# Optimization experiments

Hardware: AMD Instinct MI355X
Metric: run time of the kernel (lower is better)

## Reference

```python
import jax, jax.numpy as jnp
import numpy as np

N, E, IN, ED, HID, HEADS, OUT, G = 50000, 800000, 128, 16, 32, 4, 64, 64
NEG_SLOPE = 0.2


def gat_conv(x, src, dst, edge_attr, W, att_src, att_dst, We, att_edge, bias,
             heads, out_ch, concat):
    """PyG-style GATConv with edge attributes and mean-filled self loops.
    src/dst already include self loops; edge_attr already includes fill rows."""
    n = x.shape[0]
    h = (x @ W).reshape(n, heads, out_ch)                      # [N,H,C]
    a_src = jnp.einsum('nhc,hc->nh', h, att_src)               # [N,H]
    a_dst = jnp.einsum('nhc,hc->nh', h, att_dst)
    eh = (edge_attr @ We).reshape(-1, heads, out_ch)           # [E',H,C]
    a_edge = jnp.einsum('ehc,hc->eh', eh, att_edge)            # [E',H]
    alpha = jax.nn.leaky_relu(a_src[src] + a_dst[dst] + a_edge, NEG_SLOPE)
    # segment softmax over incoming edges of each target node
    amax = jax.ops.segment_max(alpha, dst, num_segments=n)
    ex = jnp.exp(alpha - amax[dst])
    denom = jax.ops.segment_sum(ex, dst, num_segments=n)
    coef = ex / (denom[dst] + 1e-16)                           # [E',H]
    msg = h[src] * coef[:, :, None]                            # [E',H,C]
    out = jax.ops.segment_sum(msg, dst, num_segments=n)        # [N,H,C]
    out = out.reshape(n, heads * out_ch) if concat else out.mean(axis=1)
    return out + bias


def add_self_loops(edge_index, edge_attr, n):
    loop = jnp.arange(n, dtype=edge_index.dtype)
    src = jnp.concatenate([edge_index[0], loop])
    dst = jnp.concatenate([edge_index[1], loop])
    fill = jnp.broadcast_to(edge_attr.mean(axis=0), (n, edge_attr.shape[1]))
    ea = jnp.concatenate([edge_attr, fill], axis=0)
    return src, dst, ea


def setup_inputs() -> dict:
    key = jax.random.key(0)
    ks = jax.random.split(key, 16)
    s1 = 1.0 / np.sqrt(IN)
    s2 = 1.0 / np.sqrt(HID * HEADS)
    se = 1.0 / np.sqrt(ED)
    return {
        'x': jax.random.normal(ks[0], (N, IN), jnp.float32),
        'edge_index': jax.random.randint(ks[1], (2, E), 0, N, jnp.int64),
        'edge_attr': jax.random.normal(ks[2], (E, ED), jnp.float32),
        'batch': jnp.sort(jax.random.randint(ks[3], (N,), 0, G, jnp.int64)),
        # layer 1 params (heads=4, concat=True)
        'W1': jax.random.normal(ks[4], (IN, HEADS * HID), jnp.float32) * s1,
        'att_src1': jax.random.normal(ks[5], (HEADS, HID), jnp.float32) * s1,
        'att_dst1': jax.random.normal(ks[6], (HEADS, HID), jnp.float32) * s1,
        'We1': jax.random.normal(ks[7], (ED, HEADS * HID), jnp.float32) * se,
        'att_edge1': jax.random.normal(ks[8], (HEADS, HID), jnp.float32) * se,
        'b1': jnp.zeros((HEADS * HID,), jnp.float32),
        # layer 2 params (heads=1, concat=False)
        'W2': jax.random.normal(ks[9], (HEADS * HID, OUT), jnp.float32) * s2,
        'att_src2': jax.random.normal(ks[10], (1, OUT), jnp.float32) * s2,
        'att_dst2': jax.random.normal(ks[11], (1, OUT), jnp.float32) * s2,
        'We2': jax.random.normal(ks[12], (ED, OUT), jnp.float32) * se,
        'att_edge2': jax.random.normal(ks[13], (1, OUT), jnp.float32) * se,
        'b2': jnp.zeros((OUT,), jnp.float32),
    }


def reference(x, edge_index, edge_attr, batch,
              W1, att_src1, att_dst1, We1, att_edge1, b1,
              W2, att_src2, att_dst2, We2, att_edge2, b2):
    src, dst, ea = add_self_loops(edge_index, edge_attr, x.shape[0])
    h = gat_conv(x, src, dst, ea, W1, att_src1, att_dst1, We1, att_edge1, b1,
                 HEADS, HID, concat=True)
    h = jax.nn.elu(h)
    h = gat_conv(h, src, dst, ea, W2, att_src2, att_dst2, We2, att_edge2, b2,
                 1, OUT, concat=False)
    # global mean pool over graphs
    sums = jax.ops.segment_sum(h, batch, num_segments=G)
    cnts = jax.ops.segment_sum(jnp.ones((h.shape[0],), h.dtype), batch, num_segments=G)
    return sums / jnp.maximum(cnts, 1.0)[:, None]
```

## Files before the change

kernel.cpp:

```cpp
#include <hip/hip_runtime.h>
#include <hip/hip_fp16.h>
#include <math.h>

#define NN 50000
#define NE 800000
#define EDF 16
#define C1 128
#define HID 32
#define OUTF 64
#define NG 64
#define SLOPE 0.2f
#define NB 196
#define MAXE 256
#define PB 256
#define PCH 196
#define SEB 512
#define HB 3125
#define GB1 1564

static inline int cdiv(long a, long b){ return (int)((a + b - 1) / b); }

__device__ __forceinline__ float lrelu(float x){ return x >= 0.f ? x : SLOPE * x; }

__global__ __launch_bounds__(256) void k_pre(const float* __restrict__ ea,
                                             float* __restrict__ part,
                                             const int* __restrict__ dst,
                                             int* __restrict__ deg,
                                             int* __restrict__ rank){
  int b = blockIdx.x;
  int t = threadIdx.x;
  if (b < SEB){
    const float4* ea4 = (const float4*)ea;
    const long total = (long)NE * 4;
    const long stride = (long)SEB * 256;
    float4 acc = make_float4(0.f, 0.f, 0.f, 0.f);
    for (long i = (long)b * 256 + t; i < total; i += stride * 4){
      float4 a0 = make_float4(0,0,0,0), a1 = a0, a2 = a0, a3 = a0;
      long i1 = i + stride, i2 = i + 2*stride, i3 = i + 3*stride;
      a0 = ea4[i];
      if (i1 < total) a1 = ea4[i1];
      if (i2 < total) a2 = ea4[i2];
      if (i3 < total) a3 = ea4[i3];
      acc.x += a0.x + a1.x + a2.x + a3.x;
      acc.y += a0.y + a1.y + a2.y + a3.y;
      acc.z += a0.z + a1.z + a2.z + a3.z;
      acc.w += a0.w + a1.w + a2.w + a3.w;
    }
    __shared__ float4 sp[256];
    sp[t] = acc;
    __syncthreads();
    for (int st = 128; st >= 4; st >>= 1){
      if (t < st){
        sp[t].x += sp[t+st].x; sp[t].y += sp[t+st].y;
        sp[t].z += sp[t+st].z; sp[t].w += sp[t+st].w;
      }
      __syncthreads();
    }
    if (t < 4) *(float4*)&part[b * 16 + t * 4] = sp[t];
  } else {
    long e = (long)(b - SEB) * 256 + t;
    if (e < NE) rank[e] = atomicAdd(&deg[dst[e]], 1);
  }
}

__global__ void k_scan1(const int* __restrict__ deg, int* __restrict__ rowStart,
                        int* __restrict__ blockSums,
                        const float* __restrict__ We1, const float* __restrict__ att_e1,
                        const float* __restrict__ We2, const float* __restrict__ att_e2,
                        const float* __restrict__ part,
                        float* __restrict__ M1, float* __restrict__ M2,
                        float* __restrict__ aeSL1, float* __restrict__ aeSL2){
  int t = threadIdx.x;
  if (blockIdx.x == NB){
    __shared__ float sMean[16];
    __shared__ float sM1p[64];
    if (t < 64){
      int h = t >> 4, d = t & 15;
      float s = 0.f;
      for (int c = 0; c < HID; c++) s += We1[d * C1 + h * HID + c] * att_e1[h * HID + c];
      M1[h * 16 + d] = s; sM1p[t] = s;
    }
    __shared__ float sM2p[16];
    if (t >= 64 && t < 80){
      int d = t - 64;
      float s = 0.f;
      for (int c = 0; c < OUTF; c++) s += We2[d * OUTF + c] * att_e2[c];
      M2[d] = s; sM2p[d] = s;
    }
    if (t >= 80 && t < 96){
      int c = t - 80;
      float s = 0.f;
      for (int b = 0; b < SEB; b++) s += part[b * 16 + c];
      sMean[c] = s * (1.0f / NE);
    }
    __syncthreads();
    if (t < 4){
      float s = 0.f;
      for (int d = 0; d < 16; d++) s += sMean[d] * sM1p[t * 16 + d];
      aeSL1[t] = s;
    }
    if (t == 4){
      float s = 0.f;
      for (int d = 0; d < 16; d++) s += sMean[d] * sM2p[d];
      *aeSL2 = s;
    }
    return;
  }
  __shared__ int sd[256];
  int i = blockIdx.x * 256 + t;
  int v = (i < NN) ? deg[i] : 0;
  sd[t] = v;
  __syncthreads();
  for (int off = 1; off < 256; off <<= 1){
    int add = (t >= off) ? sd[t - off] : 0;
    __syncthreads();
    sd[t] += add;
    __syncthreads();
  }
  int incl = sd[t];
  if (i < NN) rowStart[i] = incl - v;
  if (t == 255) blockSums[blockIdx.x] = incl;
}

__global__ void k_scan3(int* __restrict__ rowStart, const int* __restrict__ blockSums){
  __shared__ int sp[256];
  int t = threadIdx.x;
  int bid = blockIdx.x;
  sp[t] = (t < bid) ? blockSums[t] : 0;
  __syncthreads();
  for (int st = 128; st >= 1; st >>= 1){
    if (t < st) sp[t] += sp[t + st];
    __syncthreads();
  }
  int prefix = sp[0];
  int i = bid * 256 + t;
  if (i < NN) rowStart[i] += prefix;
  if (i == 0) rowStart[NN] = NE;
}

__global__ __launch_bounds__(256) void k_sg(
    const int* __restrict__ src, const int* __restrict__ dst,
    const float* __restrict__ ea, const int* __restrict__ rowStart,
    const int* __restrict__ rank,
    const float* __restrict__ M1, const float* __restrict__ M2,
    unsigned int* __restrict__ recC,
    const float* __restrict__ A, const float* __restrict__ B,
    __half* __restrict__ Ch, const float* __restrict__ attS,
    const float* __restrict__ attD,
    float* __restrict__ aS, float* __restrict__ aD){
  __shared__ float As[16][64];
  __shared__ float Bs[16][64];
  __shared__ float sM[80];
  int t = threadIdx.x;
  if (blockIdx.x >= GB1){
    if (t < 64) sM[t] = M1[t];
    if (t >= 64 && t < 80) sM[t] = M2[t - 64];
    __syncthreads();
    long e = (long)(blockIdx.x - GB1) * 256 + t;
    if (e >= NE) return;
    int d = dst[e];
    int s = src[e];
    int rk = rank[e];
    float eav[16];
    const float4* p = (const float4*)(ea + e * EDF);
    *(float4*)&eav[0]  = p[0]; *(float4*)&eav[4]  = p[1];
    *(float4*)&eav[8]  = p[2]; *(float4*)&eav[12] = p[3];
    int pos = rowStart[d] + rk;
    float ae[4];
#pragma unroll
    for (int h = 0; h < 4; h++){
      float sdot = 0.f;
#pragma unroll
      for (int dd = 0; dd < 16; dd++) sdot += eav[dd] * sM[h * 16 + dd];
      ae[h] = sdot;
    }
    float a2 = 0.f;
#pragma unroll
    for (int dd = 0; dd < 16; dd++) a2 += eav[dd] * sM[64 + dd];
    __half2 ae01 = __floats2half2_rn(ae[0], ae[1]);
    __half2 ae23 = __floats2half2_rn(ae[2], ae[3]);
    __half  a2h  = __float2half_rn(a2);
    uint4 rec;
    rec.x = (unsigned)s | ((unsigned)*(unsigned short*)&a2h << 16);
    rec.y = *(unsigned*)&ae01;
    rec.z = *(unsigned*)&ae23;
    rec.w = 0u;
    *(uint4*)&recC[(long)pos * 4] = rec;
    return;
  }
  const int M = NN, Ncols = C1, K = 128;
  int bg = blockIdx.x;
  int row0 = (bg >> 1) * 64, col0 = (bg & 1) * 64;
  int tx = t & 15, ty = t >> 4;
  int lrow = t >> 2, lkq = t & 3;
  int bk = t >> 4, bc = t & 15;
  float acc[4][4] = {};
  for (int k0 = 0; k0 < K; k0 += 16){
    float4 a4 = make_float4(0.f, 0.f, 0.f, 0.f);
    int gr = row0 + lrow;
    if (gr < M) a4 = *(const float4*)&A[(long)gr * K + k0 + lkq * 4];
    As[lkq * 4 + 0][lrow] = a4.x; As[lkq * 4 + 1][lrow] = a4.y;
    As[lkq * 4 + 2][lrow] = a4.z; As[lkq * 4 + 3][lrow] = a4.w;
    *(float4*)&Bs[bk][bc * 4] = *(const float4*)&B[(long)(k0 + bk) * Ncols + col0 + bc * 4];
    __syncthreads();
#pragma unroll
    for (int k = 0; k < 16; k++){
      float4 a = *(float4*)&As[k][ty * 4];
      float4 b = *(float4*)&Bs[k][tx * 4];
      acc[0][0] += a.x*b.x; acc[0][1] += a.x*b.y; acc[0][2] += a.x*b.z; acc[0][3] += a.x*b.w;
      acc[1][0] += a.y*b.x; acc[1][1] += a.y*b.y; acc[1][2] += a.y*b.z; acc[1][3] += a.y*b.w;
      acc[2][0] += a.z*b.x; acc[2][1] += a.z*b.y; acc[2][2] += a.z*b.z; acc[2][3] += a.z*b.w;
      acc[3][0] += a.w*b.x; acc[3][1] += a.w*b.y; acc[3][2] += a.w*b.z; acc[3][3] += a.w*b.w;
    }
    __syncthreads();
  }
#pragma unroll
  for (int i = 0; i < 4; i++){
    int r = row0 + ty * 4 + i;
    if (r < M){
      __half2 p0 = __floats2half2_rn(acc[i][0], acc[i][1]);
      __half2 p1 = __floats2half2_rn(acc[i][2], acc[i][3]);
      uint2 pk; pk.x = *(unsigned*)&p0; pk.y = *(unsigned*)&p1;
      *(uint2*)&Ch[(long)r * Ncols + col0 + tx * 4] = pk;
    }
  }
  float4 avS = *(const float4*)&attS[col0 + tx * 4];
  float4 avD = *(const float4*)&attD[col0 + tx * 4];
  float ss[4], sd[4];
#pragma unroll
  for (int i = 0; i < 4; i++){
    ss[i] = acc[i][0]*avS.x + acc[i][1]*avS.y + acc[i][2]*avS.z + acc[i][3]*avS.w;
    sd[i] = acc[i][0]*avD.x + acc[i][1]*avD.y + acc[i][2]*avD.z + acc[i][3]*avD.w;
  }
#pragma unroll
  for (int off = 1; off <= 4; off <<= 1){
#pragma unroll
    for (int i = 0; i < 4; i++){
      ss[i] += __shfl_xor(ss[i], off);
      sd[i] += __shfl_xor(sd[i], off);
    }
  }
  if ((tx & 7) == 0){
    int head = (bg & 1) * 2 + (tx >> 3);
#pragma unroll
    for (int i = 0; i < 4; i++){
      int r = row0 + ty * 4 + i;
      if (r < M){ aS[(long)r * 4 + head] = ss[i]; aD[(long)r * 4 + head] = sd[i]; }
    }
  }
}

__global__ __launch_bounds__(256) void k_gemm2(const __half* __restrict__ Ah,
                                               const float* __restrict__ B,
                                               __half* __restrict__ Ch,
                                               const float* __restrict__ attS,
                                               const float* __restrict__ attD,
                                               float* __restrict__ aS, float* __restrict__ aD){
  __shared__ float As[16][64];
  __shared__ float Bs[16][64];
  const int M = NN, Ncols = OUTF, K = 128;
  int tid = threadIdx.x;
  int row0 = blockIdx.x * 64, col0 = 0;
  int tx = tid & 15, ty = tid >> 4;
  int lrow = tid >> 2, lkq = tid & 3;
  int bk = tid >> 4, bc = tid & 15;
  float acc[4][4] = {};
  for (int k0 = 0; k0 < K; k0 += 16){
    float4 a4 = make_float4(0.f, 0.f, 0.f, 0.f);
    int gr = row0 + lrow;
    if (gr < M){
      uint2 u = *(const uint2*)&Ah[(long)gr * K + k0 + lkq * 4];
      float2 f0 = __half22float2(*(__half2*)&u.x);
      float2 f1 = __half22float2(*(__half2*)&u.y);
      a4 = make_float4(f0.x, f0.y, f1.x, f1.y);
    }
    As[lkq * 4 + 0][lrow] = a4.x; As[lkq * 4 + 1][lrow] = a4.y;
    As[lkq * 4 + 2][lrow] = a4.z; As[lkq * 4 + 3][lrow] = a4.w;
    *(float4*)&Bs[bk][bc * 4] = *(const float4*)&B[(long)(k0 + bk) * Ncols + col0 + bc * 4];
    __syncthreads();
#pragma unroll
    for (int k = 0; k < 16; k++){
      float4 a = *(float4*)&As[k][ty * 4];
      float4 b = *(float4*)&Bs[k][tx * 4];
      acc[0][0] += a.x*b.x; acc[0][1] += a.x*b.y; acc[0][2] += a.x*b.z; acc[0][3] += a.x*b.w;
      acc[1][0] += a.y*b.x; acc[1][1] += a.y*b.y; acc[1][2] += a.y*b.z; acc[1][3] += a.y*b.w;
      acc[2][0] += a.z*b.x; acc[2][1] += a.z*b.y; acc[2][2] += a.z*b.z; acc[2][3] += a.z*b.w;
      acc[3][0] += a.w*b.x; acc[3][1] += a.w*b.y; acc[3][2] += a.w*b.z; acc[3][3] += a.w*b.w;
    }
    __syncthreads();
  }
#pragma unroll
  for (int i = 0; i < 4; i++){
    int r = row0 + ty * 4 + i;
    if (r < M){
      __half2 p0 = __floats2half2_rn(acc[i][0], acc[i][1]);
      __half2 p1 = __floats2half2_rn(acc[i][2], acc[i][3]);
      uint2 pk; pk.x = *(unsigned*)&p0; pk.y = *(unsigned*)&p1;
      *(uint2*)&Ch[(long)r * Ncols + tx * 4] = pk;
    }
  }
  float4 avS = *(const float4*)&attS[tx * 4];
  float4 avD = *(const float4*)&attD[tx * 4];
  float ss[4], sd[4];
#pragma unroll
  for (int i = 0; i < 4; i++){
    ss[i] = acc[i][0]*avS.x + acc[i][1]*avS.y + acc[i][2]*avS.z + acc[i][3]*avS.w;
    sd[i] = acc[i][0]*avD.x + acc[i][1]*avD.y + acc[i][2]*avD.z + acc[i][3]*avD.w;
  }
#pragma unroll
  for (int off = 1; off <= 8; off <<= 1){
#pragma unroll
    for (int i = 0; i < 4; i++){
      ss[i] += __shfl_xor(ss[i], off);
      sd[i] += __shfl_xor(sd[i], off);
    }
  }
  if (tx == 0){
#pragma unroll
    for (int i = 0; i < 4; i++){
      int r = row0 + ty * 4 + i;
      if (r < M){ aS[r] = ss[i]; aD[r] = sd[i]; }
    }
  }
}

__global__ __launch_bounds__(256) void k_agg1(
    const int* __restrict__ rowStart, const unsigned int* __restrict__ recC,
    const float* __restrict__ a_src, const float* __restrict__ a_dst,
    const float* __restrict__ aeSL1,
    const __half* __restrict__ h1h, const float* __restrict__ b1,
    __half* __restrict__ out1h){
  __shared__ int   sS[4][MAXE];
  __shared__ float sC[4][MAXE * 4];
  int wid = threadIdx.x >> 6;
  int lane = threadIdx.x & 63;
  int n = blockIdx.x * 4 + wid;
  int start = rowStart[n];
  int dg = rowStart[n + 1] - start;
  float4 sl4 = *(const float4*)aeSL1;
  float4 ad4 = *(const float4*)(a_dst + (long)n * 4);
  float4 as4 = *(const float4*)(a_src + (long)n * 4);
  float4 cSelf;
  cSelf.x = __expf(lrelu(as4.x + ad4.x + sl4.x));
  cSelf.y = __expf(lrelu(as4.y + ad4.y + sl4.y));
  cSelf.z = __expf(lrelu(as4.z + ad4.z + sl4.z));
  cSelf.w = __expf(lrelu(as4.w + ad4.w + sl4.w));
  float4 dsum = make_float4(0.f, 0.f, 0.f, 0.f);
  for (int j0 = 0; j0 < dg; j0 += 64){
    int j = j0 + lane;
    if (j < dg){
      uint4 rec = *(const uint4*)&recC[(long)(start + j) * 4];
      int s = rec.x & 0xffff;
      float2 ae01 = __half22float2(*(__half2*)&rec.y);
      float2 ae23 = __half22float2(*(__half2*)&rec.z);
      float4 asv = *(const float4*)(a_src + (long)s * 4);
      float4 c;
      c.x = __expf(lrelu(asv.x + ad4.x + ae01.x));
      c.y = __expf(lrelu(asv.y + ad4.y + ae01.y));
      c.z = __expf(lrelu(asv.z + ad4.z + ae23.x));
      c.w = __expf(lrelu(asv.w + ad4.w + ae23.y));
      dsum.x += c.x; dsum.y += c.y; dsum.z += c.z; dsum.w += c.w;
      if (j < MAXE){
        sS[wid][j] = s << 6;
        *(float4*)&sC[wid][j * 4] = c;
      }
    }
  }
#pragma unroll
  for (int off = 32; off > 0; off >>= 1){
    dsum.x += __shfl_xor(dsum.x, off);
    dsum.y += __shfl_xor(dsum.y, off);
    dsum.z += __shfl_xor(dsum.z, off);
    dsum.w += __shfl_xor(dsum.w, off);
  }
  float adA[4] = {ad4.x, ad4.y, ad4.z, ad4.w};
  float csA[4] = {cSelf.x, cSelf.y, cSelf.z, cSelf.w};
  float invA[4];
  invA[0] = 1.f / (dsum.x + cSelf.x + 1e-16f);
  invA[1] = 1.f / (dsum.y + cSelf.y + 1e-16f);
  invA[2] = 1.f / (dsum.z + cSelf.z + 1e-16f);
  invA[3] = 1.f / (dsum.w + cSelf.w + 1e-16f);
  int ch = lane * 2;
  int h = lane >> 4;
  const unsigned int* hrow = (const unsigned int*)h1h;
  float cs   = csA[h];
  float vinv = invA[h];
  float adh  = adA[h];
  unsigned int hv = hrow[(unsigned)(n * 64 + lane)];
  float2 hf = __half22float2(*(__half2*)&hv);
  float acc0 = hf.x * cs, acc1 = hf.y * cs;
  int jmax = dg < MAXE ? dg : MAXE;
  int j = 0;
  for (; j + 4 <= jmax; j += 4){
    int o0 = sS[wid][j+0], o1 = sS[wid][j+1], o2 = sS[wid][j+2], o3 = sS[wid][j+3];
    float c0 = sC[wid][(j+0)*4+h], c1 = sC[wid][(j+1)*4+h];
    float c2 = sC[wid][(j+2)*4+h], c3 = sC[wid][(j+3)*4+h];
    unsigned int v0 = hrow[(unsigned)(o0 + lane)];
    unsigned int v1 = hrow[(unsigned)(o1 + lane)];
    unsigned int v2 = hrow[(unsigned)(o2 + lane)];
    unsigned int v3 = hrow[(unsigned)(o3 + lane)];
    float2 f0 = __half22float2(*(__half2*)&v0);
    float2 f1 = __half22float2(*(__half2*)&v1);
    float2 f2 = __half22float2(*(__half2*)&v2);
    float2 f3 = __half22float2(*(__half2*)&v3);
    acc0 += c0 * f0.x + c1 * f1.x + c2 * f2.x + c3 * f3.x;
    acc1 += c0 * f0.y + c1 * f1.y + c2 * f2.y + c3 * f3.y;
  }
  for (; j < jmax; j++){
    int o = sS[wid][j];
    float c = sC[wid][j * 4 + h];
    unsigned int v = hrow[(unsigned)(o + lane)];
    float2 f = __half22float2(*(__half2*)&v);
    acc0 += c * f.x; acc1 += c * f.y;
  }
  for (; j < dg; j++){
    uint4 rec = *(const uint4*)&recC[(long)(start + j) * 4];
    int s = rec.x & 0xffff;
    float2 ae01 = __half22float2(*(__half2*)&rec.y);
    float2 ae23 = __half22float2(*(__half2*)&rec.z);
    float aeA[4] = {ae01.x, ae01.y, ae23.x, ae23.y};
    float asv = a_src[(long)s * 4 + h];
    float c = __expf(lrelu(asv + adh + aeA[h]));
    unsigned int v = hrow[(unsigned)((s << 6) + lane)];
    float2 f = __half22float2(*(__half2*)&v);
    acc0 += c * f.x; acc1 += c * f.y;
  }
  float v0 = acc0 * vinv + b1[ch];
  float v1 = acc1 * vinv + b1[ch + 1];
  v0 = v0 > 0.f ? v0 : __expf(v0) - 1.f;
  v1 = v1 > 0.f ? v1 : __expf(v1) - 1.f;
  __half2 pk = __floats2half2_rn(v0, v1);
  ((unsigned int*)out1h)[(unsigned)(n * 64 + lane)] = *(unsigned*)&pk;
}

__global__ __launch_bounds__(256) void k_agg2(
    const int* __restrict__ rowStart, const unsigned int* __restrict__ recC,
    const float* __restrict__ a_src, const float* __restrict__ a_dst,
    const float* __restrict__ aeSL2,
    const __half* __restrict__ h2h, float* __restrict__ out2){
  __shared__ int   sS[4][MAXE];
  __shared__ float sC[4][MAXE];
  int wid = threadIdx.x >> 6;
  int lane = threadIdx.x & 63;
  int n = blockIdx.x * 4 + wid;
  int start = rowStart[n];
  int dg = rowStart[n + 1] - start;
  float adN = a_dst[n];
  float cSelf = __expf(lrelu(a_src[n] + adN + *aeSL2));
  float dsum = 0.f;
  for (int j0 = 0; j0 < dg; j0 += 64){
    int j = j0 + lane;
    if (j < dg){
      unsigned rx = recC[(long)(start + j) * 4];
      int s = rx & 0xffff;
      unsigned short ah = (unsigned short)(rx >> 16);
      float c = __expf(lrelu(a_src[s] + adN + __half2float(*(__half*)&ah)));
      dsum += c;
      if (j < MAXE){ sS[wid][j] = s << 6; sC[wid][j] = c; }
    }
  }
#pragma unroll
  for (int off = 32; off > 0; off >>= 1) dsum += __shfl_xor(dsum, off);
  float inv = 1.f / (dsum + cSelf + 1e-16f);
  float acc = __half2float(h2h[(unsigned)(n * 64 + lane)]) * cSelf;
  int jmax = dg < MAXE ? dg : MAXE;
  int j = 0;
  for (; j + 4 <= jmax; j += 4){
    int o0 = sS[wid][j+0], o1 = sS[wid][j+1], o2 = sS[wid][j+2], o3 = sS[wid][j+3];
    float c0 = sC[wid][j+0], c1 = sC[wid][j+1], c2 = sC[wid][j+2], c3 = sC[wid][j+3];
    float f0 = __half2float(h2h[(unsigned)(o0 + lane)]);
    float f1 = __half2float(h2h[(unsigned)(o1 + lane)]);
    float f2 = __half2float(h2h[(unsigned)(o2 + lane)]);
    float f3 = __half2float(h2h[(unsigned)(o3 + lane)]);
    acc += c0 * f0 + c1 * f1 + c2 * f2 + c3 * f3;
  }
  for (; j < jmax; j++)
    acc += sC[wid][j] * __half2float(h2h[(unsigned)(sS[wid][j] + lane)]);
  for (; j < dg; j++){
    unsigned rx = recC[(long)(start + j) * 4];
    int s = rx & 0xffff;
    unsigned short ah = (unsigned short)(rx >> 16);
    float c = __expf(lrelu(a_src[s] + adN + __half2float(*(__half*)&ah)));
    acc += c * __half2float(h2h[(unsigned)((s << 6) + lane)]);
  }
  out2[(long)n * OUTF + lane] = acc * inv;
}

__global__ __launch_bounds__(256) void k_pool1(const float* __restrict__ out2,
                                               const int* __restrict__ batch,
                                               float* __restrict__ gsum){
  int c = threadIdx.x & 63, r = threadIdx.x >> 6;
  int n0 = blockIdx.x * PCH + r;
  int n1 = blockIdx.x * PCH + PCH; if (n1 > NN) n1 = NN;
  float acc = 0.f; int curG = -1;
  for (int n = n0; n < n1; n += 4){
    int g = batch[n];
    if (g != curG){
      if (curG >= 0) atomicAdd(&gsum[curG * 64 + c], acc);
      curG = g; acc = 0.f;
    }
    acc += out2[(long)n * OUTF + c];
  }
  if (curG >= 0) atomicAdd(&gsum[curG * 64 + c], acc);
}

__global__ void k_pool2(const float* __restrict__ gsum, const int* __restrict__ batch,
                        const float* __restrict__ b2, float* __restrict__ out){
  int g = blockIdx.x;
  int c = threadIdx.x;
  int lo = 0, hi = NN;
  while (lo < hi){ int mid = (lo + hi) >> 1; if (batch[mid] < g) lo = mid + 1; else hi = mid; }
  int a = lo, b = NN;
  while (a < b){ int mid = (a + b) >> 1; if (batch[mid] < g + 1) a = mid + 1; else b = mid; }
  int cnt = a - lo;
  out[g * 64 + c] = (gsum[g * 64 + c] + (float)cnt * b2[c]) / fmaxf((float)cnt, 1.0f);
}

extern "C" void kernel_launch(void* const* d_in, const int* in_sizes, int n_in,
                              void* d_out, int out_size, void* d_ws, size_t ws_size,
                              hipStream_t stream) {
  const float* x         = (const float*)d_in[0];
  const int*   eidx      = (const int*)d_in[1];
  const float* edge_attr = (const float*)d_in[2];
  const int*   batch     = (const int*)d_in[3];
  const float* W1        = (const float*)d_in[4];
  const float* att_src1  = (const float*)d_in[5];
  const float* att_dst1  = (const float*)d_in[6];
  const float* We1       = (const float*)d_in[7];
  const float* att_edge1 = (const float*)d_in[8];
  const float* b1        = (const float*)d_in[9];
  const float* W2        = (const float*)d_in[10];
  const float* att_src2  = (const float*)d_in[11];
  const float* att_dst2  = (const float*)d_in[12];
  const float* We2       = (const float*)d_in[13];
  const float* att_edge2 = (const float*)d_in[14];
  const float* b2        = (const float*)d_in[15];
  const int* srcI = eidx;
  const int* dstI = eidx + NE;

  float* ws = (float*)d_ws;
  __half* h1h   = (__half*)ws;
  __half* out1h = (__half*)(ws + 3200000);
  float* out2   = ws + 6400000;
  float* a_src1 = ws + 9600000;
  float* a_dst1 = a_src1 + (long)NN * 4;
  unsigned int* recC = (unsigned int*)(a_dst1 + (long)NN * 4);
  int*   deg    = (int*)(recC + (long)NE * 4);
  float* gsum   = (float*)(deg + NN);
  int*   rowStart = (int*)(gsum + NG * 64);
  int*   blockSums = rowStart + 50004;
  float* part   = (float*)(blockSums + 260);
  float* M1     = part + SEB * 16;
  float* M2v    = M1 + 64;
  float* aeSL1  = M2v + 16;
  float* aeSL2  = aeSL1 + 4;
  int*   rank   = (int*)(aeSL2 + 4);
  __half* h2h = h1h;
  float* a_src2 = a_src1; float* a_dst2 = a_dst1;

  hipMemsetAsync(deg, 0, (NN + NG * 64) * sizeof(int), stream);
  k_pre<<<SEB + HB, 256, 0, stream>>>(edge_attr, part, dstI, deg, rank);
  k_scan1<<<NB + 1, 256, 0, stream>>>(deg, rowStart, blockSums,
                                      We1, att_edge1, We2, att_edge2, part,
                                      M1, M2v, aeSL1, aeSL2);
  k_scan3<<<NB, 256, 0, stream>>>(rowStart, blockSums);
  k_sg<<<GB1 + HB, 256, 0, stream>>>(srcI, dstI, edge_attr, rowStart, rank,
                                     M1, M2v, recC,
                                     x, W1, h1h, att_src1, att_dst1,
                                     a_src1, a_dst1);
  k_agg1<<<NN / 4, 256, 0, stream>>>(rowStart, recC, a_src1, a_dst1, aeSL1,
                                     h1h, b1, out1h);
  k_gemm2<<<dim3(cdiv(NN, 64), 1), 256, 0, stream>>>(out1h, W2, h2h, att_src2, att_dst2,
                                                     a_src2, a_dst2);
  k_agg2<<<NN / 4, 256, 0, stream>>>(rowStart, recC, a_src2, a_dst2, aeSL2,
                                     h2h, out2);
  k_pool1<<<PB, 256, 0, stream>>>(out2, batch, gsum);
  k_pool2<<<NG, 64, 0, stream>>>(gsum, batch, b2, (float*)d_out);
}
```

Baseline: 330.7 us.

## Use split-fp16 MFMA for both GAT GEMMs and separate edge-scatter kernel

Replaces the scalar fp32 SIMT GEMMs for layer 1 and layer 2 with MFMA 16x16x32 fp16 kernels. Precision is kept near fp32 by splitting operands into high and scaled low fp16 parts: three products for layer 1, two for layer 2. Weights are pre-transposed and split in extra blocks of the scan kernel, and the attention logits are fused into the GEMM epilogue. The edge record scatter previously fused with GEMM1 becomes its own kernel launch, which removes that concurrency and adds some rounding-error risk.

New measurement: 352.6 us. +6.6%, slower.

```diff
diff --git a/kernel.cpp b/kernel.cpp
--- a/kernel.cpp
+++ b/kernel.cpp
@@ -16,11 +16,16 @@
 #define PCH 196
 #define SEB 512
 #define HB 3125
-#define GB1 1564
+#define G1B 1563
+#define G2B 1563
 
 static inline int cdiv(long a, long b){ return (int)((a + b - 1) / b); }
 
 __device__ __forceinline__ float lrelu(float x){ return x >= 0.f ? x : SLOPE * x; }
+
+typedef _Float16 f16x8 __attribute__((ext_vector_type(8)));
+typedef float f32x4 __attribute__((ext_vector_type(4)));
+#define MFMA16(a, b, c) __builtin_amdgcn_mfma_f32_16x16x32_f16((a), (b), (c), 0, 0, 0)
 
 __global__ __launch_bounds__(256) void k_pre(const float* __restrict__ ea,
                                              float* __restrict__ part,
@@ -69,8 +74,31 @@
                         const float* __restrict__ We2, const float* __restrict__ att_e2,
                         const float* __restrict__ part,
                         float* __restrict__ M1, float* __restrict__ M2,
-                        float* __restrict__ aeSL1, float* __restrict__ aeSL2){
+                        float* __restrict__ aeSL1, float* __restrict__ aeSL2,
+                        const float* __restrict__ W1, const float* __restrict__ W2,
+                        __half* __restrict__ W1Th, __half* __restrict__ W1Tl,
+                        __half* __restrict__ W2Th, __half* __restrict__ W2Tl){
   int t = threadIdx.x;
+  if (blockIdx.x == NB + 1){
+    for (int i = t; i < 128 * 128; i += 256){
+      int c = i & 127, k = i >> 7;
+      float w = W1[i];
+      __half h = __float2half_rn(w);
+      W1Th[c * 128 + k] = h;
+      W1Tl[c * 128 + k] = __float2half_rn((w - __half2float(h)) * 4096.0f);
+    }
+    return;
+  }
+  if (blockIdx.x == NB + 2){
+    for (int i = t; i < 128 * 64; i += 256){
+      int c = i & 63, k = i >> 6;
+      float w = W2[i];
+      __half h = __float2half_rn(w);
+      W2Th[c * 128 + k] = h;
+      W2Tl[c * 128 + k] = __float2half_rn((w - __half2float(h)) * 4096.0f);
+    }
+    return;
+  }
   if (blockIdx.x == NB){
     __shared__ float sMean[16];
     __shared__ float sM1p[64];
@@ -138,189 +166,259 @@
   if (i == 0) rowStart[NN] = NE;
 }
 
-__global__ __launch_bounds__(256) void k_sg(
+__global__ __launch_bounds__(256) void k_gemm1(
+    const float* __restrict__ x,
+    const __half* __restrict__ W1Th, const __half* __restrict__ W1Tl,
+    __half* __restrict__ Ch,
+    const float* __restrict__ attS, const float* __restrict__ attD,
+    float* __restrict__ aS, float* __restrict__ aD){
+  __shared__ __align__(16) __half Ash[4096];
+  __shared__ __align__(16) __half Asl[4096];
+  int t = threadIdx.x;
+  int row0 = blockIdx.x * 32;
+  {
+    int srow = t >> 3, sseg = t & 7;
+    int gr = row0 + srow;
+    float xv[16];
+    if (gr < NN){
+      const float4* xp = (const float4*)(x + (long)gr * 128 + sseg * 16);
+      *(float4*)&xv[0]  = xp[0]; *(float4*)&xv[4]  = xp[1];
+      *(float4*)&xv[8]  = xp[2]; *(float4*)&xv[12] = xp[3];
+    } else {
+#pragma unroll
+      for (int i = 0; i < 16; i++) xv[i] = 0.f;
+    }
+    f16x8 vh[2], vl[2];
+#pragma unroll
+    for (int q = 0; q < 2; q++)
+#pragma unroll
+      for (int i = 0; i < 8; i++){
+        float f = xv[q * 8 + i];
+        _Float16 h = (_Float16)f;
+        vh[q][i] = h;
+        vl[q][i] = (_Float16)(f - (float)h);
+      }
+    int sb = srow * 256 + sseg * 32;
+    int sw = (srow & 7) << 4;
+    *(f16x8*)((char*)Ash + ((sb     ) ^ sw)) = vh[0];
+    *(f16x8*)((char*)Ash + ((sb + 16) ^ sw)) = vh[1];
+    *(f16x8*)((char*)Asl + ((sb     ) ^ sw)) = vl[0];
+    *(f16x8*)((char*)Asl + ((sb + 16) ^ sw)) = vl[1];
+  }
+  __syncthreads();
+  int wave = t >> 6, lane = t & 63, g = lane >> 4, li = lane & 15;
+  const f16x8* BhP = (const f16x8*)W1Th;
+  const f16x8* BlP = (const f16x8*)W1Tl;
+  int c0 = wave * 32 + li;
+  int c1 = c0 + 16;
+  f32x4 z = {0.f, 0.f, 0.f, 0.f};
+  f32x4 aM00 = z, aM01 = z, aM10 = z, aM11 = z;
+  f32x4 aL00 = z, aL01 = z, aL10 = z, aL11 = z;
+  int ro0 = li * 256, ro1 = (16 + li) * 256;
+  int sw0 = (li & 7) << 4;
+#pragma unroll
+  for (int ks = 0; ks < 4; ks++){
+    int ko = ks * 64 + g * 16;
+    f16x8 ah0 = *(const f16x8*)((char*)Ash + ((ro0 + ko) ^ sw0));
+    f16x8 ah1 = *(const f16x8*)((char*)Ash + ((ro1 + ko) ^ sw0));
+    f16x8 al0 = *(const f16x8*)((char*)Asl + ((ro0 + ko) ^ sw0));
+    f16x8 al1 = *(const f16x8*)((char*)Asl + ((ro1 + ko) ^ sw0));
+    f16x8 bh0 = BhP[c0 * 16 + ks * 4 + g];
+    f16x8 bh1 = BhP[c1 * 16 + ks * 4 + g];
+    f16x8 bl0 = BlP[c0 * 16 + ks * 4 + g];
+    f16x8 bl1 = BlP[c1 * 16 + ks * 4 + g];
+    aM00 = MFMA16(ah0, bh0, aM00); aM01 = MFMA16(ah0, bh1, aM01);
+    aM10 = MFMA16(ah1, bh0, aM10); aM11 = MFMA16(ah1, bh1, aM11);
+    aM00 = MFMA16(al0, bh0, aM00); aM01 = MFMA16(al0, bh1, aM01);
+    aM10 = MFMA16(al1, bh0, aM10); aM11 = MFMA16(al1, bh1, aM11);
+    aL00 = MFMA16(ah0, bl0, aL00); aL01 = MFMA16(ah0, bl1, aL01);
+    aL10 = MFMA16(ah1, bl0, aL10); aL11 = MFMA16(ah1, bl1, aL11);
+  }
+  const float s = 1.0f / 4096.0f;
+  f32x4 D00 = aM00 + aL00 * s, D01 = aM01 + aL01 * s;
+  f32x4 D10 = aM10 + aL10 * s, D11 = aM11 + aL11 * s;
+  float avS0 = attS[c0], avS1 = attS[c1];
+  float avD0 = attD[c0], avD1 = attD[c1];
+  float ssv[2][4], sdv[2][4];
+#pragma unroll
+  for (int r = 0; r < 4; r++){
+    ssv[0][r] = D00[r] * avS0 + D01[r] * avS1;
+    ssv[1][r] = D10[r] * avS0 + D11[r] * avS1;
+    sdv[0][r] = D00[r] * avD0 + D01[r] * avD1;
+    sdv[1][r] = D10[r] * avD0 + D11[r] * avD1;
+  }
+#pragma unroll
+  for (int off = 1; off <= 8; off <<= 1)
+#pragma unroll
+    for (int mt = 0; mt < 2; mt++)
+#pragma unroll
+      for (int r = 0; r < 4; r++){
+        ssv[mt][r] += __shfl_xor(ssv[mt][r], off);
+        sdv[mt][r] += __shfl_xor(sdv[mt][r], off);
+      }
+  __syncthreads();
+  __half* sOut = Ash;
+#pragma unroll
+  for (int mt = 0; mt < 2; mt++)
+#pragma unroll
+    for (int r = 0; r < 4; r++){
+      int rl = mt * 16 + g * 4 + r;
+      sOut[rl * 128 + c0] = __float2half_rn(mt ? D10[r] : D00[r]);
+      sOut[rl * 128 + c1] = __float2half_rn(mt ? D11[r] : D01[r]);
+    }
+  if (li == 0){
+#pragma unroll
+    for (int mt = 0; mt < 2; mt++)
+#pragma unroll
+      for (int r = 0; r < 4; r++){
+        int grow = row0 + mt * 16 + g * 4 + r;
+        if (grow < NN){
+          aS[(long)grow * 4 + wave] = ssv[mt][r];
+          aD[(long)grow * 4 + wave] = sdv[mt][r];
+        }
+      }
+  }
+  __syncthreads();
+  {
+    int row = t >> 3, seg = t & 7;
+    int grw = row0 + row;
+    if (grw < NN){
+      uint4 u0 = *(uint4*)&sOut[row * 128 + seg * 16];
+      uint4 u1 = *(uint4*)&sOut[row * 128 + seg * 16 + 8];
+      *(uint4*)&Ch[(long)grw * 128 + seg * 16] = u0;
+      *(uint4*)&Ch[(long)grw * 128 + seg * 16 + 8] = u1;
+    }
+  }
+}
+
+__global__ __launch_bounds__(256) void k_sc(
     const int* __restrict__ src, const int* __restrict__ dst,
     const float* __restrict__ ea, const int* __restrict__ rowStart,
     const int* __restrict__ rank,
     const float* __restrict__ M1, const float* __restrict__ M2,
-    unsigned int* __restrict__ recC,
-    const float* __restrict__ A, const float* __restrict__ B,
-    __half* __restrict__ Ch, const float* __restrict__ attS,
-    const float* __restrict__ attD,
-    float* __restrict__ aS, float* __restrict__ aD){
-  __shared__ float As[16][64];
-  __shared__ float Bs[16][64];
+    unsigned int* __restrict__ recC){
   __shared__ float sM[80];
   int t = threadIdx.x;
-  if (blockIdx.x >= GB1){
-    if (t < 64) sM[t] = M1[t];
-    if (t >= 64 && t < 80) sM[t] = M2[t - 64];
-    __syncthreads();
-    long e = (long)(blockIdx.x - GB1) * 256 + t;
-    if (e >= NE) return;
-    int d = dst[e];
-    int s = src[e];
-    int rk = rank[e];
-    float eav[16];
-    const float4* p = (const float4*)(ea + e * EDF);
-    *(float4*)&eav[0]  = p[0]; *(float4*)&eav[4]  = p[1];
-    *(float4*)&eav[8]  = p[2]; *(float4*)&eav[12] = p[3];
-    int pos = rowStart[d] + rk;
-    float ae[4];
-#pragma unroll
-    for (int h = 0; h < 4; h++){
-      float sdot = 0.f;
-#pragma unroll
-      for (int dd = 0; dd < 16; dd++) sdot += eav[dd] * sM[h * 16 + dd];
-      ae[h] = sdot;
-    }
-    float a2 = 0.f;
-#pragma unroll
-    for (int dd = 0; dd < 16; dd++) a2 += eav[dd] * sM[64 + dd];
-    __half2 ae01 = __floats2half2_rn(ae[0], ae[1]);
-    __half2 ae23 = __floats2half2_rn(ae[2], ae[3]);
-    __half  a2h  = __float2half_rn(a2);
-    uint4 rec;
-    rec.x = (unsigned)s | ((unsigned)*(unsigned short*)&a2h << 16);
-    rec.y = *(unsigned*)&ae01;
-    rec.z = *(unsigned*)&ae23;
-    rec.w = 0u;
-    *(uint4*)&recC[(long)pos * 4] = rec;
-    return;
-  }
-  const int M = NN, Ncols = C1, K = 128;
-  int bg = blockIdx.x;
-  int row0 = (bg >> 1) * 64, col0 = (bg & 1) * 64;
-  int tx = t & 15, ty = t >> 4;
-  int lrow = t >> 2, lkq = t & 3;
-  int bk = t >> 4, bc = t & 15;
-  float acc[4][4] = {};
-  for (int k0 = 0; k0 < K; k0 += 16){
-    float4 a4 = make_float4(0.f, 0.f, 0.f, 0.f);
-    int gr = row0 + lrow;
-    if (gr < M) a4 = *(const float4*)&A[(long)gr * K + k0 + lkq * 4];
-    As[lkq * 4 + 0][lrow] = a4.x; As[lkq * 4 + 1][lrow] = a4.y;
-    As[lkq * 4 + 2][lrow] = a4.z; As[lkq * 4 + 3][lrow] = a4.w;
-    *(float4*)&Bs[bk][bc * 4] = *(const float4*)&B[(long)(k0 + bk) * Ncols + col0 + bc * 4];
-    __syncthreads();
-#pragma unroll
-    for (int k = 0; k < 16; k++){
-      float4 a = *(float4*)&As[k][ty * 4];
-      float4 b = *(float4*)&Bs[k][tx * 4];
-      acc[0][0] += a.x*b.x; acc[0][1] += a.x*b.y; acc[0][2] += a.x*b.z; acc[0][3] += a.x*b.w;
-      acc[1][0] += a.y*b.x; acc[1][1] += a.y*b.y; acc[1][2] += a.y*b.z; acc[1][3] += a.y*b.w;
-      acc[2][0] += a.z*b.x; acc[2][1] += a.z*b.y; acc[2][2] += a.z*b.z; acc[2][3] += a.z*b.w;
-      acc[3][0] += a.w*b.x; acc[3][1] += a.w*b.y; acc[3][2] += a.w*b.z; acc[3][3] += a.w*b.w;
-    }
-    __syncthreads();
-  }
-#pragma unroll
-  for (int i = 0; i < 4; i++){
-    int r = row0 + ty * 4 + i;
-    if (r < M){
-      __half2 p0 = __floats2half2_rn(acc[i][0], acc[i][1]);
-      __half2 p1 = __floats2half2_rn(acc[i][2], acc[i][3]);
-      uint2 pk; pk.x = *(unsigned*)&p0; pk.y = *(unsigned*)&p1;
-      *(uint2*)&Ch[(long)r * Ncols + col0 + tx * 4] = pk;
-    }
-  }
-  float4 avS = *(const float4*)&attS[col0 + tx * 4];
-  float4 avD = *(const float4*)&attD[col0 + tx * 4];
-  float ss[4], sd[4];
-#pragma unroll
-  for (int i = 0; i < 4; i++){
-    ss[i] = acc[i][0]*avS.x + acc[i][1]*avS.y + acc[i][2]*avS.z + acc[i][3]*avS.w;
-    sd[i] = acc[i][0]*avD.x + acc[i][1]*avD.y + acc[i][2]*avD.z + acc[i][3]*avD.w;
-  }
-#pragma unroll
-  for (int off = 1; off <= 4; off <<= 1){
-#pragma unroll
-    for (int i = 0; i < 4; i++){
-      ss[i] += __shfl_xor(ss[i], off);
-      sd[i] += __shfl_xor(sd[i], off);
-    }
-  }
-  if ((tx & 7) == 0){
-    int head = (bg & 1) * 2 + (tx >> 3);
-#pragma unroll
-    for (int i = 0; i < 4; i++){
-      int r = row0 + ty * 4 + i;
-      if (r < M){ aS[(long)r * 4 + head] = ss[i]; aD[(long)r * 4 + head] = sd[i]; }
-    }
-  }
-}
-
-__global__ __launch_bounds__(256) void k_gemm2(const __half* __restrict__ Ah,
-                                               const float* __restrict__ B,
-                                               __half* __restrict__ Ch,
-                                               const float* __restrict__ attS,
-                                               const float* __restrict__ attD,
-                                               float* __restrict__ aS, float* __restrict__ aD){
-  __shared__ float As[16][64];
-  __shared__ float Bs[16][64];
-  const int M = NN, Ncols = OUTF, K = 128;
-  int tid = threadIdx.x;
-  int row0 = blockIdx.x * 64, col0 = 0;
-  int tx = tid & 15, ty = tid >> 4;
-  int lrow = tid >> 2, lkq = tid & 3;
-  int bk = tid >> 4, bc = tid & 15;
-  float acc[4][4] = {};
-  for (int k0 = 0; k0 < K; k0 += 16){
-    float4 a4 = make_float4(0.f, 0.f, 0.f, 0.f);
-    int gr = row0 + lrow;
-    if (gr < M){
-      uint2 u = *(const uint2*)&Ah[(long)gr * K + k0 + lkq * 4];
-      float2 f0 = __half22float2(*(__half2*)&u.x);
-      float2 f1 = __half22float2(*(__half2*)&u.y);
-      a4 = make_float4(f0.x, f0.y, f1.x, f1.y);
-    }
-    As[lkq * 4 + 0][lrow] = a4.x; As[lkq * 4 + 1][lrow] = a4.y;
-    As[lkq * 4 + 2][lrow] = a4.z; As[lkq * 4 + 3][lrow] = a4.w;
-    *(float4*)&Bs[bk][bc * 4] = *(const float4*)&B[(long)(k0 + bk) * Ncols + col0 + bc * 4];
-    __syncthreads();
-#pragma unroll
-    for (int k = 0; k < 16; k++){
-      float4 a = *(float4*)&As[k][ty * 4];
-      float4 b = *(float4*)&Bs[k][tx * 4];
-      acc[0][0] += a.x*b.x; acc[0][1] += a.x*b.y; acc[0][2] += a.x*b.z; acc[0][3] += a.x*b.w;
-      acc[1][0] += a.y*b.x; acc[1][1] += a.y*b.y; acc[1][2] += a.y*b.z; acc[1][3] += a.y*b.w;
-      acc[2][0] += a.z*b.x; acc[2][1] += a.z*b.y; acc[2][2] += a.z*b.z; acc[2][3] += a.z*b.w;
-      acc[3][0] += a.w*b.x; acc[3][1] += a.w*b.y; acc[3][2] += a.w*b.z; acc[3][3] += a.w*b.w;
-    }
-    __syncthreads();
-  }
-#pragma unroll
-  for (int i = 0; i < 4; i++){
-    int r = row0 + ty * 4 + i;
-    if (r < M){
-      __half2 p0 = __floats2half2_rn(acc[i][0], acc[i][1]);
-      __half2 p1 = __floats2half2_rn(acc[i][2], acc[i][3]);
-      uint2 pk; pk.x = *(unsigned*)&p0; pk.y = *(unsigned*)&p1;
-      *(uint2*)&Ch[(long)r * Ncols + tx * 4] = pk;
-    }
-  }
-  float4 avS = *(const float4*)&attS[tx * 4];
-  float4 avD = *(const float4*)&attD[tx * 4];
-  float ss[4], sd[4];
-#pragma unroll
-  for (int i = 0; i < 4; i++){
-    ss[i] = acc[i][0]*avS.x + acc[i][1]*avS.y + acc[i][2]*avS.z + acc[i][3]*avS.w;
-    sd[i] = acc[i][0]*avD.x + acc[i][1]*avD.y + acc[i][2]*avD.z + acc[i][3]*avD.w;
-  }
-#pragma unroll
-  for (int off = 1; off <= 8; off <<= 1){
-#pragma unroll
-    for (int i = 0; i < 4; i++){
-      ss[i] += __shfl_xor(ss[i], off);
-      sd[i] += __shfl_xor(sd[i], off);
-    }
-  }
-  if (tx == 0){
-#pragma unroll
-    for (int i = 0; i < 4; i++){
-      int r = row0 + ty * 4 + i;
-      if (r < M){ aS[r] = ss[i]; aD[r] = sd[i]; }
-    }
+  if (t < 64) sM[t] = M1[t];
+  if (t >= 64 && t < 80) sM[t] = M2[t - 64];
+  __syncthreads();
+  long e = (long)blockIdx.x * 256 + t;
+  if (e >= NE) return;
+  int d = dst[e];
+  int s = src[e];
+  int rk = rank[e];
+  float eav[16];
+  const float4* p = (const float4*)(ea + e * EDF);
+  *(float4*)&eav[0]  = p[0]; *(float4*)&eav[4]  = p[1];
+  *(float4*)&eav[8]  = p[2]; *(float4*)&eav[12] = p[3];
+  int pos = rowStart[d] + rk;
+  float ae[4];
+#pragma unroll
+  for (int h = 0; h < 4; h++){
+    float sdot = 0.f;
+#pragma unroll
+    for (int dd = 0; dd < 16; dd++) sdot += eav[dd] * sM[h * 16 + dd];
+    ae[h] = sdot;
+  }
+  float a2 = 0.f;
+#pragma unroll
+  for (int dd = 0; dd < 16; dd++) a2 += eav[dd] * sM[64 + dd];
+  __half2 ae01 = __floats2half2_rn(ae[0], ae[1]);
+  __half2 ae23 = __floats2half2_rn(ae[2], ae[3]);
+  __half  a2h  = __float2half_rn(a2);
+  uint4 rec;
+  rec.x = (unsigned)s | ((unsigned)*(unsigned short*)&a2h << 16);
+  rec.y = *(unsigned*)&ae01;
+  rec.z = *(unsigned*)&ae23;
+  rec.w = 0u;
+  *(uint4*)&recC[(long)pos * 4] = rec;
+}
+
+__global__ __launch_bounds__(256) void k_gemm2(
+    const __half* __restrict__ Ahp,
+    const __half* __restrict__ W2Th, const __half* __restrict__ W2Tl,
+    __half* __restrict__ Ch,
+    const float* __restrict__ attS, const float* __restrict__ attD,
+    float* __restrict__ aS, float* __restrict__ aD){
+  __shared__ __align__(16) __half As[4096];
+  __shared__ float sRS[128], sRD[128];
+  int t = threadIdx.x;
+  int row0 = blockIdx.x * 32;
+  {
+    int srow = t >> 3, sseg = t & 7;
+    int gr = row0 + srow;
+    uint4 u0 = {0,0,0,0}, u1 = {0,0,0,0};
+    if (gr < NN){
+      const uint4* p = (const uint4*)(Ahp + (long)gr * 128 + sseg * 16);
+      u0 = p[0]; u1 = p[1];
+    }
+    int sb = srow * 256 + sseg * 32;
+    int sw = (srow & 7) << 4;
+    *(uint4*)((char*)As + ((sb     ) ^ sw)) = u0;
+    *(uint4*)((char*)As + ((sb + 16) ^ sw)) = u1;
+  }
+  __syncthreads();
+  int wave = t >> 6, lane = t & 63, g = lane >> 4, li = lane & 15;
+  int cw = wave * 16 + li;
+  const f16x8* BhP = (const f16x8*)W2Th;
+  const f16x8* BlP = (const f16x8*)W2Tl;
+  f32x4 z = {0.f, 0.f, 0.f, 0.f};
+  f32x4 aM0 = z, aM1 = z, aL0 = z, aL1 = z;
+  int ro0 = li * 256, ro1 = (16 + li) * 256, sw0 = (li & 7) << 4;
+#pragma unroll
+  for (int ks = 0; ks < 4; ks++){
+    int ko = ks * 64 + g * 16;
+    f16x8 a0 = *(const f16x8*)((char*)As + ((ro0 + ko) ^ sw0));
+    f16x8 a1 = *(const f16x8*)((char*)As + ((ro1 + ko) ^ sw0));
+    f16x8 bh = BhP[cw * 16 + ks * 4 + g];
+    f16x8 bl = BlP[cw * 16 + ks * 4 + g];
+    aM0 = MFMA16(a0, bh, aM0); aM1 = MFMA16(a1, bh, aM1);
+    aL0 = MFMA16(a0, bl, aL0); aL1 = MFMA16(a1, bl, aL1);
+  }
+  const float s = 1.0f / 4096.0f;
+  f32x4 D0 = aM0 + aL0 * s, D1 = aM1 + aL1 * s;
+  float avS = attS[cw], avD = attD[cw];
+  float ssv[2][4], sdv[2][4];
+#pragma unroll
+  for (int r = 0; r < 4; r++){
+    ssv[0][r] = D0[r] * avS; ssv[1][r] = D1[r] * avS;
+    sdv[0][r] = D0[r] * avD; sdv[1][r] = D1[r] * avD;
+  }
+#pragma unroll
+  for (int off = 1; off <= 8; off <<= 1)
+#pragma unroll
+    for (int mt = 0; mt < 2; mt++)
+#pragma unroll
+      for (int r = 0; r < 4; r++){
+        ssv[mt][r] += __shfl_xor(ssv[mt][r], off);
+        sdv[mt][r] += __shfl_xor(sdv[mt][r], off);
+      }
+  __syncthreads();
+  __half* sOut = As;
+#pragma unroll
+  for (int mt = 0; mt < 2; mt++)
+#pragma unroll
+    for (int r = 0; r < 4; r++){
+      int rl = mt * 16 + g * 4 + r;
+      sOut[rl * 64 + cw] = __float2half_rn(mt ? D1[r] : D0[r]);
+      if (li == 0){
+        sRS[wave * 32 + rl] = ssv[mt][r];
+        sRD[wave * 32 + rl] = sdv[mt][r];
+      }
+    }
+  __syncthreads();
+  if (t < 32){
+    int grow = row0 + t;
+    if (grow < NN){
+      aS[grow] = sRS[t] + sRS[32 + t] + sRS[64 + t] + sRS[96 + t];
+      aD[grow] = sRD[t] + sRD[32 + t] + sRD[64 + t] + sRD[96 + t];
+    }
+  }
+  {
+    int row = t >> 3, seg = t & 7;
+    int grw = row0 + row;
+    if (grw < NN)
+      *(uint4*)&Ch[(long)grw * 64 + seg * 8] = *(uint4*)&sOut[row * 64 + seg * 8];
   }
 }
 
@@ -555,23 +653,28 @@
   float* aeSL1  = M2v + 16;
   float* aeSL2  = aeSL1 + 4;
   int*   rank   = (int*)(aeSL2 + 4);
+  __half* W1Th  = (__half*)(rank + NE);
+  __half* W1Tl  = W1Th + 16384;
+  __half* W2Th  = W1Tl + 16384;
+  __half* W2Tl  = W2Th + 8192;
   __half* h2h = h1h;
   float* a_src2 = a_src1; float* a_dst2 = a_dst1;
 
   hipMemsetAsync(deg, 0, (NN + NG * 64) * sizeof(int), stream);
   k_pre<<<SEB + HB, 256, 0, stream>>>(edge_attr, part, dstI, deg, rank);
-  k_scan1<<<NB + 1, 256, 0, stream>>>(deg, rowStart, blockSums,
+  k_scan1<<<NB + 3, 256, 0, stream>>>(deg, rowStart, blockSums,
                                       We1, att_edge1, We2, att_edge2, part,
-                                      M1, M2v, aeSL1, aeSL2);
+                                      M1, M2v, aeSL1, aeSL2,
+                                      W1, W2, W1Th, W1Tl, W2Th, W2Tl);
   k_scan3<<<NB, 256, 0, stream>>>(rowStart, blockSums);
-  k_sg<<<GB1 + HB, 256, 0, stream>>>(srcI, dstI, edge_attr, rowStart, rank,
-                                     M1, M2v, recC,
-                                     x, W1, h1h, att_src1, att_dst1,
-                                     a_src1, a_dst1);
+  k_gemm1<<<G1B, 256, 0, stream>>>(x, W1Th, W1Tl, h1h, att_src1, att_dst1,
+                                   a_src1, a_dst1);
+  k_sc<<<HB, 256, 0, stream>>>(srcI, dstI, edge_attr, rowStart, rank,
+                               M1, M2v, recC);
   k_agg1<<<NN / 4, 256, 0, stream>>>(rowStart, recC, a_src1, a_dst1, aeSL1,
                                      h1h, b1, out1h);
-  k_gemm2<<<dim3(cdiv(NN, 64), 1), 256, 0, stream>>>(out1h, W2, h2h, att_src2, att_dst2,
-                                                     a_src2, a_dst2);
+  k_gemm2<<<G2B, 256, 0, stream>>>(out1h, W2Th, W2Tl, h2h, att_src2, att_dst2,
+                                   a_src2, a_dst2);
   k_agg2<<<NN / 4, 256, 0, stream>>>(rowStart, recC, a_src2, a_dst2, aeSL2,
                                      h2h, out2);
   k_pool1<<<PB, 256, 0, stream>>>(out2, batch, gsum);
```
